# Kernel tuning notes

Hardware: AMD Instinct MI355X
Metric: run time of the kernel (lower is better)

The kernel has to match this reference:

```python
import jax, jax.numpy as jnp
import numpy as np

B, D, L = 32, 512, 4096   # batch, latent_dim (dim1), time length
N, D2 = 77, 768           # text tokens, text_latent_dim (dim2)
BC = 24                   # number of conditioned batch elements
H = 8                     # num_heads
EPS = 1e-5


def _layernorm(x, g, b):
    mu = jnp.mean(x, axis=-1, keepdims=True)
    var = jnp.mean(jnp.square(x - mu), axis=-1, keepdims=True)
    return (x - mu) * jax.lax.rsqrt(var + EPS) * g + b


def setup_inputs() -> dict:
    key = jax.random.key(0)
    ks = jax.random.split(key, 8)
    s = 0.02
    return {
        "input_tensor": jax.random.normal(ks[0], (B, D, L), jnp.float32),
        "condition_tensor": jax.random.normal(ks[1], (B, N, D2), jnp.float32),
        "cond_indices": jnp.arange(BC, dtype=jnp.int64 if jax.config.jax_enable_x64 else jnp.int32),
        "ln_g": jnp.ones((D,), jnp.float32),
        "ln_b": jnp.zeros((D,), jnp.float32),
        "tln_g": jnp.ones((D2,), jnp.float32),
        "tln_b": jnp.zeros((D2,), jnp.float32),
        "Wq": jax.random.normal(ks[2], (D, D), jnp.float32) * s,
        "bq": jnp.zeros((D,), jnp.float32),
        "Wk": jax.random.normal(ks[3], (D2, D), jnp.float32) * s,
        "bk": jnp.zeros((D,), jnp.float32),
        "Wv": jax.random.normal(ks[4], (D2, D), jnp.float32) * s,
        "bv": jnp.zeros((D,), jnp.float32),
    }


def reference(input_tensor, condition_tensor, cond_indices,
              ln_g, ln_b, tln_g, tln_b, Wq, bq, Wk, bk, Wv, bv):
    dh = D // H
    # gather conditioned rows; [Bc, D, L] -> [Bc, T=L, D]
    x_cond = jnp.transpose(input_tensor[cond_indices], (0, 2, 1))
    cond = condition_tensor[cond_indices]  # [Bc, N, D2]

    q = _layernorm(x_cond, ln_g, ln_b) @ Wq + bq           # [Bc, T, D]
    cn = _layernorm(cond, tln_g, tln_b)                     # [Bc, N, D2]
    k = (cn @ Wk + bk).reshape(BC, N, H, dh)
    v = (cn @ Wv + bv).reshape(BC, N, H, dh)

    q = jax.nn.softmax(q.reshape(BC, L, H, dh), axis=-1)   # feature-map softmax
    k = jax.nn.softmax(k, axis=1)                           # softmax over tokens N

    context = jnp.einsum('bnhk,bnhv->bhkv', k, v)           # [Bc, H, dh, dh]
    y = jnp.einsum('bthk,bhkv->bthv', q, context).reshape(BC, L, D)

    # scatter residual back: indices are unique, so .add == torch index assignment
    return input_tensor.at[cond_indices].add(jnp.transpose(y, (0, 2, 1)))
```

## Files before the change

kernel.cpp:

```cpp
#include <hip/hip_runtime.h>

#define LN_EPS 1e-5f

typedef __attribute__((ext_vector_type(8))) short bf16x8;
typedef __attribute__((ext_vector_type(4))) float f32x4;

__device__ __forceinline__ unsigned short f2bf(float f){
  unsigned u = __builtin_bit_cast(unsigned, f);
  u = (u + 0x7fffu + ((u >> 16) & 1u)) >> 16;
  return (unsigned short)u;
}
__device__ __forceinline__ float bf2f(unsigned short h){
  unsigned u = ((unsigned)h) << 16;
  return __builtin_bit_cast(float, u);
}

__global__ void k_prep(const float* __restrict__ Wq, const float* __restrict__ ln_g,
                       const float* __restrict__ ln_b, const float* __restrict__ bq,
                       unsigned short* __restrict__ gWqT, float2* __restrict__ c12)
{
  __shared__ float r1[64][4], r2[64][4];
  const int tid = threadIdx.x;
  const int n0 = blockIdx.x * 64;
  const int c = tid & 63, q = tid >> 6;
  const int n = n0 + c;
  float c1p = 0.f, c2p = 0.f;
  for(int i=0;i<128;i+=4){
    ushort4 pk;
    unsigned short* pp = (unsigned short*)&pk;
    #pragma unroll
    for(int j=0;j<4;j++){
      const int d = q*128 + i + j;
      const float wv = Wq[(size_t)d*512 + n];
      const unsigned short hb = f2bf(ln_g[d] * wv);
      pp[j] = hb;
      c2p += bf2f(hb);
      c1p += ln_b[d] * wv;
    }
    *(ushort4*)(gWqT + (size_t)n*512 + q*128 + i) = pk;
  }
  r1[c][q] = c1p; r2[c][q] = c2p;
  __syncthreads();
  if(q == 0){
    float a = 0.f, b2 = 0.f;
    #pragma unroll
    for(int j=0;j<4;j++){ a += r1[c][j]; b2 += r2[c][j]; }
    c12[n] = make_float2(a + bq[n], b2);
  }
}

__global__ void k_condkv(const float* __restrict__ cond, const int* __restrict__ idx,
                         const float* __restrict__ tg, const float* __restrict__ tb,
                         const float* __restrict__ Wk, const float* __restrict__ bk,
                         const float* __restrict__ Wv, const float* __restrict__ bv,
                         float* __restrict__ kbuf, float* __restrict__ vbuf)
{
  __shared__ float cn[16][768];
  const int bc = blockIdx.z, nc = blockIdx.y, dc = blockIdx.x;
  const int b = idx[bc];
  const int n0 = nc * 16;
  int nrows = 77 - n0; if(nrows > 16) nrows = 16;
  const int w = threadIdx.x >> 6, lane = threadIdx.x & 63;

  for(int r = w; r < nrows; r += 4){
    const float* src = cond + ((size_t)b * 77 + n0 + r) * 768;
    float vals[12]; float s1 = 0.f, s2 = 0.f;
    #pragma unroll
    for(int i=0;i<12;i++){ float x = src[lane + i*64]; vals[i]=x; s1+=x; s2+=x*x; }
    #pragma unroll
    for(int off=1; off<64; off<<=1){ s1 += __shfl_xor(s1, off); s2 += __shfl_xor(s2, off); }
    const float mu  = s1 * (1.f/768.f);
    const float var = s2 * (1.f/768.f) - mu*mu;
    const float rs  = rsqrtf(var + LN_EPS);
    #pragma unroll
    for(int i=0;i<12;i++){ const int c2 = lane + i*64; cn[r][c2] = (vals[i]-mu)*rs*tg[c2] + tb[c2]; }
  }
  __syncthreads();

  const int dq = threadIdx.x & 63;
  const int part = threadIdx.x >> 6;
  const float* W    = (dc < 2) ? Wk : Wv;
  const float* bias = (dc < 2) ? bk : bv;
  float* obuf       = (dc < 2) ? kbuf : vbuf;
  const int d0 = (dc & 1) * 256 + dq * 4;

  float acc[4][4] = {};
  for(int i=0;i<768;i++){
    const float4 wv = *(const float4*)(W + (size_t)i * 512 + d0);
    #pragma unroll
    for(int j=0;j<4;j++){
      const float c = cn[part*4 + j][i];
      acc[j][0] += c * wv.x; acc[j][1] += c * wv.y;
      acc[j][2] += c * wv.z; acc[j][3] += c * wv.w;
    }
  }
  #pragma unroll
  for(int j=0;j<4;j++){
    const int r = part*4 + j, n = n0 + r;
    if(r < nrows){
      float4 o;
      o.x = acc[j][0] + bias[d0+0];
      o.y = acc[j][1] + bias[d0+1];
      o.z = acc[j][2] + bias[d0+2];
      o.w = acc[j][3] + bias[d0+3];
      *(float4*)(obuf + ((size_t)bc * 77 + n) * 512 + d0) = o;
    }
  }
}

__global__ void k_ctx(const float* __restrict__ kbuf, const float* __restrict__ vbuf,
                      unsigned short* __restrict__ ctxP)
{
  __shared__ float kk[77][64];
  __shared__ float vv[77][64];
  __shared__ float inv_s[64];
  const int h = blockIdx.x, bc = blockIdx.y;
  const int tid = threadIdx.x;
  for(int e = tid; e < 77*64; e += 256){
    const int n = e >> 6, c = e & 63;
    kk[n][c] = kbuf[((size_t)bc * 77 + n) * 512 + h*64 + c];
    vv[n][c] = vbuf[((size_t)bc * 77 + n) * 512 + h*64 + c];
  }
  __syncthreads();
  if(tid < 64){
    float m = -1e30f;
    for(int n=0;n<77;n++) m = fmaxf(m, kk[n][tid]);
    float s = 0.f;
    for(int n=0;n<77;n++){ const float e = __expf(kk[n][tid] - m); kk[n][tid] = e; s += e; }
    inv_s[tid] = 1.f / s;
  }
  __syncthreads();
  #pragma unroll
  for(int j=0;j<16;j++){
    const int o = tid + 256*j;
    const int v = o >> 6, k2 = o & 63;
    float a = 0.f;
    for(int n=0;n<77;n++) a += kk[n][k2] * vv[n][v];
    const int pos = ((((k2>>5)*4 + (v>>4))*4 + ((k2>>3)&3))*16 + (v&15))*8 + (k2&7);
    ctxP[((size_t)(bc*8 + h)) * 4096 + pos] = f2bf(a * inv_s[k2]);
  }
}

__global__ __launch_bounds__(256, 3)
void k_fused(const float* __restrict__ input, const int* __restrict__ idx,
             const unsigned short* __restrict__ gWqT, const float2* __restrict__ c12,
             const unsigned short* __restrict__ ctxP, float* __restrict__ out)
{
  const int nt  = blockIdx.x;
  const int by  = blockIdx.y;
  const int tid = threadIdx.x;

  if(by >= 1536){
    const int cid = (by - 1536)*2 + nt;
    const int nb = cid >> 6, chunk = cid & 63;
    int cnt = 0, bsel = 0;
    for(int b2 = 0; b2 < 32; ++b2){
      bool member = false;
      #pragma unroll
      for(int i2 = 0; i2 < 24; ++i2) member |= (idx[i2] == b2);
      if(!member){ if(cnt == nb) bsel = b2; ++cnt; }
    }
    const float4* s = (const float4*)(input + (size_t)bsel * 2097152) + chunk*8192;
    float4*       d = (float4*)      (out   + (size_t)bsel * 2097152) + chunk*8192;
    #pragma unroll
    for(int i = 0; i < 32; ++i) d[i*256 + tid] = s[i*256 + tid];
    return;
  }

  __shared__ __align__(16) char smem[40960];
  unsigned short* const P = (unsigned short*)smem;
  float* const mu_s = (float*)(smem + 37376);
  float* const rs_s = (float*)(smem + 37632);
  float* const red1 = (float*)(smem + 37888);
  float* const red2 = (float*)(smem + 38912);

  const int lane = tid & 63, w = tid >> 6;
  const int col = lane & 15, g = lane >> 4;
  const int bc = by >> 6, b = idx[bc];
  const int t0 = (by & 63) * 64;
  const int nbase = nt * 256;
  const float* xb = input + (size_t)b * 2097152;

  const int tq = tid & 15;
  const int kb = tid >> 4;
  const float* xsrc = xb + (size_t)(kb*2) * 4096 + t0 + tq*4;

  int wx[4];
  #pragma unroll
  for(int j=0;j<4;j++){
    const int t = tq*4 + j;
    wx[j] = t*64 + ((((kb>>2) ^ ((t>>1)&3)) & 3) << 4) + ((kb & 3) << 2);
  }
  int offA[4];
  #pragma unroll
  for(int mt=0; mt<4; ++mt){
    const int row = mt*16 + col;
    offA[mt] = row*64 + ((g ^ ((row>>1)&3)) << 4);
  }
  const char* wrow[4];
  #pragma unroll
  for(int ntl=0; ntl<4; ++ntl)
    wrow[ntl] = (const char*)gWqT + (size_t)(nbase + w*64 + ntl*16 + col)*1024 + g*16;

  #define PUTX(ya, yb2, Xd)                                           \
  { _Pragma("unroll")                                                 \
    for(int j=0;j<4;j++)                                              \
      *(ushort2*)((Xd) + wx[j]) = make_ushort2(f2bf((&(ya).x)[j]), f2bf((&(yb2).x)[j])); }
  #define STATS(ya, yb2)                                              \
  { _Pragma("unroll")                                                 \
    for(int j=0;j<4;j++){                                             \
      const float a_ = (&(ya).x)[j], b_ = (&(yb2).x)[j];              \
      s1[j] += a_ + b_; s2[j] += a_*a_ + b_*b_; } }

  float s1[4] = {0,0,0,0}, s2[4] = {0,0,0,0};
  f32x4 acc[4][4] = {};

  {
    float4 xa  = *(const float4*)(xsrc);
    float4 xb2 = *(const float4*)(xsrc + 4096);
    STATS(xa, xb2);
    PUTX(xa, xb2, smem);
  }
  __syncthreads();

  for(int ks = 0; ks < 16; ++ks){
    char* const Xc = smem + ((ks & 1) << 12);
    char* const Xn = smem + (((ks + 1) & 1) << 12);
    float4 xa, xb2;
    const bool pf = (ks < 15);
    if(pf){
      xa  = *(const float4*)(xsrc + (size_t)((ks+1)*32) * 4096);
      xb2 = *(const float4*)(xsrc + (size_t)((ks+1)*32 + 1) * 4096);
    }
    bf16x8 bfr[4], af[4];
    #pragma unroll
    for(int ntl=0; ntl<4; ++ntl) bfr[ntl] = *(const bf16x8*)(wrow[ntl] + ks*64);
    #pragma unroll
    for(int mt=0; mt<4; ++mt) af[mt] = *(const bf16x8*)(Xc + offA[mt]);
    #pragma unroll
    for(int mt=0; mt<4; ++mt)
      #pragma unroll
      for(int ntl=0; ntl<4; ++ntl)
        acc[mt][ntl] = __builtin_amdgcn_mfma_f32_16x16x32_bf16(af[mt], bfr[ntl], acc[mt][ntl], 0, 0, 0);
    if(pf){
      STATS(xa, xb2);
      PUTX(xa, xb2, Xn);
    }
    __syncthreads();
  }
  #undef PUTX
  #undef STATS

  #pragma unroll
  for(int j=0;j<4;j++){
    s1[j] += __shfl_xor(s1[j], 16); s2[j] += __shfl_xor(s2[j], 16);
    s1[j] += __shfl_xor(s1[j], 32); s2[j] += __shfl_xor(s2[j], 32);
  }
  if(lane < 16){
    #pragma unroll
    for(int j=0;j<4;j++){
      red1[(lane*4 + j)*4 + w] = s1[j];
      red2[(lane*4 + j)*4 + w] = s2[j];
    }
  }
  __syncthreads();
  if(tid < 64){
    float a = 0.f, c = 0.f;
    #pragma unroll
    for(int ww=0; ww<4; ++ww){ a += red1[tid*4 + ww]; c += red2[tid*4 + ww]; }
    const float mu  = a * (1.f/512.f);
    const float var = c * (1.f/512.f) - mu*mu;
    mu_s[tid] = mu;
    rs_s[tid] = rsqrtf(var + LN_EPS);
  }
  __syncthreads();

  const int head = nt*4 + w;
  float c1b[4], c2v[4];
  #pragma unroll
  for(int ntl=0; ntl<4; ++ntl){
    const float2 cc = c12[nbase + w*64 + ntl*16 + col];
    c1b[ntl] = cc.x;
    c2v[ntl] = cc.y;
  }
  #pragma unroll
  for(int mt=0; mt<4; ++mt){
    #pragma unroll
    for(int r=0; r<4; ++r){
      const int tl = mt*16 + g*4 + r;
      const float rsr = rs_s[tl];
      const float mrc = rsr * mu_s[tl];
      float v[4];
      #pragma unroll
      for(int ntl=0; ntl<4; ++ntl)
        v[ntl] = rsr*acc[mt][ntl][r] - mrc*c2v[ntl] + c1b[ntl];
      float m = fmaxf(fmaxf(v[0],v[1]), fmaxf(v[2],v[3]));
      m = fmaxf(m, __shfl_xor(m, 1));
      m = fmaxf(m, __shfl_xor(m, 2));
      m = fmaxf(m, __shfl_xor(m, 4));
      m = fmaxf(m, __shfl_xor(m, 8));
      float s = 0.f;
      #pragma unroll
      for(int ntl=0; ntl<4; ++ntl){ v[ntl] = __expf(v[ntl] - m); s += v[ntl]; }
      s += __shfl_xor(s, 1);
      s += __shfl_xor(s, 2);
      s += __shfl_xor(s, 4);
      s += __shfl_xor(s, 8);
      const float inv = 1.f / s;
      #pragma unroll
      for(int ntl=0; ntl<4; ++ntl) acc[mt][ntl][r] = v[ntl] * inv;
    }
  }

  unsigned short* const Pw = P + w * (64*72);
  #pragma unroll
  for(int mt=0; mt<4; ++mt)
    #pragma unroll
    for(int ntl=0; ntl<4; ++ntl)
      #pragma unroll
      for(int r=0; r<4; ++r)
        Pw[(mt*16 + g*4 + r)*72 + ntl*16 + col] = f2bf(acc[mt][ntl][r]);

  const unsigned short* cp = ctxP + (size_t)(bc*8 + head) * 4096;
  f32x4 y[4][4] = {};
  #pragma unroll
  for(int ks2=0; ks2<2; ++ks2){
    bf16x8 pa[4];
    #pragma unroll
    for(int mt=0; mt<4; ++mt)
      pa[mt] = *(const bf16x8*)(Pw + (mt*16 + col)*72 + ks2*32 + g*8);
    bf16x8 cv[4];
    #pragma unroll
    for(int vt=0; vt<4; ++vt)
      cv[vt] = *(const bf16x8*)(cp + (size_t)(((ks2*4 + vt)*4 + g)*16 + col) * 8);
    #pragma unroll
    for(int mt=0; mt<4; ++mt)
      #pragma unroll
      for(int vt=0; vt<4; ++vt)
        y[mt][vt] = __builtin_amdgcn_mfma_f32_16x16x32_bf16(pa[mt], cv[vt], y[mt][vt], 0, 0, 0);
  }

  float* const ob = out + (size_t)b * 2097152;
  #pragma unroll
  for(int mt=0; mt<4; ++mt)
    #pragma unroll
    for(int vt=0; vt<4; ++vt){
      const size_t a = (size_t)(head*64 + vt*16 + col)*4096
                     + (size_t)(t0 + mt*16 + g*4);
      const float4 xr4 = *(const float4*)(xb + a);
      float4 o4;
      o4.x = xr4.x + y[mt][vt][0];
      o4.y = xr4.y + y[mt][vt][1];
      o4.z = xr4.z + y[mt][vt][2];
      o4.w = xr4.w + y[mt][vt][3];
      *(float4*)(ob + a) = o4;
    }
}

extern "C" void kernel_launch(void* const* d_in, const int* in_sizes, int n_in,
                              void* d_out, int out_size, void* d_ws, size_t ws_size,
                              hipStream_t stream)
{
  const float* input = (const float*)d_in[0];
  const float* cond  = (const float*)d_in[1];
  const int*   idx   = (const int*)d_in[2];
  const float* ln_g  = (const float*)d_in[3];
  const float* ln_b  = (const float*)d_in[4];
  const float* tln_g = (const float*)d_in[5];
  const float* tln_b = (const float*)d_in[6];
  const float* Wq    = (const float*)d_in[7];
  const float* bq    = (const float*)d_in[8];
  const float* Wk    = (const float*)d_in[9];
  const float* bk    = (const float*)d_in[10];
  const float* Wv    = (const float*)d_in[11];
  const float* bv    = (const float*)d_in[12];
  float* out = (float*)d_out;
  char*  ws  = (char*)d_ws;

  unsigned short* gWqT = (unsigned short*)(ws);
  float2*         c12  = (float2*)(ws + 524288);
  unsigned short* ctxP = (unsigned short*)(ws + 528384);
  float* kbuf = (float*)(ws + 2101248);
  float* vbuf = (float*)(ws + 2101248 + 3784704);

  k_prep  <<<dim3(8),       dim3(256), 0, stream>>>(Wq, ln_g, ln_b, bq, gWqT, c12);
  k_condkv<<<dim3(4,5,24),  dim3(256), 0, stream>>>(cond, idx, tln_g, tln_b, Wk, bk, Wv, bv, kbuf, vbuf);
  k_ctx   <<<dim3(8,24),    dim3(256), 0, stream>>>(kbuf, vbuf, ctxP);
  k_fused <<<dim3(2,1792),  dim3(256), 0, stream>>>(input, idx, gWqT, c12, ctxP, out);
}
```

Before: 416.6 us.

## Merge prep into cond-KV kernel and restructure fused GEMM X staging with K=64 steps

Folds the Wq preparation kernel into the cond K/V projection kernel as an extra z-slice, which removes one launch. Restructures the fused kernel's X tile loading: each thread now loads 16 scalar column elements per step, packs them into two 16-byte LDS writes with a new 8-way XOR swizzle, and processes K=64 per iteration (8 iterations instead of 16). This halves the number of barriers and lets each thread compute LN stats per row without shuffles. The trade-off is scalar strided global loads (coalesced across t) in place of float4 loads, plus a larger LDS footprint per buffer.

```diff
diff --git a/kernel.cpp b/kernel.cpp
--- a/kernel.cpp
+++ b/kernel.cpp
@@ -14,53 +14,61 @@
   unsigned u = ((unsigned)h) << 16;
   return __builtin_bit_cast(float, u);
 }
-
-__global__ void k_prep(const float* __restrict__ Wq, const float* __restrict__ ln_g,
-                       const float* __restrict__ ln_b, const float* __restrict__ bq,
-                       unsigned short* __restrict__ gWqT, float2* __restrict__ c12)
-{
-  __shared__ float r1[64][4], r2[64][4];
-  const int tid = threadIdx.x;
-  const int n0 = blockIdx.x * 64;
-  const int c = tid & 63, q = tid >> 6;
-  const int n = n0 + c;
-  float c1p = 0.f, c2p = 0.f;
-  for(int i=0;i<128;i+=4){
-    ushort4 pk;
-    unsigned short* pp = (unsigned short*)&pk;
-    #pragma unroll
-    for(int j=0;j<4;j++){
-      const int d = q*128 + i + j;
-      const float wv = Wq[(size_t)d*512 + n];
-      const unsigned short hb = f2bf(ln_g[d] * wv);
-      pp[j] = hb;
-      c2p += bf2f(hb);
-      c1p += ln_b[d] * wv;
-    }
-    *(ushort4*)(gWqT + (size_t)n*512 + q*128 + i) = pk;
-  }
-  r1[c][q] = c1p; r2[c][q] = c2p;
-  __syncthreads();
-  if(q == 0){
-    float a = 0.f, b2 = 0.f;
-    #pragma unroll
-    for(int j=0;j<4;j++){ a += r1[c][j]; b2 += r2[c][j]; }
-    c12[n] = make_float2(a + bq[n], b2);
-  }
-}
-
-__global__ void k_condkv(const float* __restrict__ cond, const int* __restrict__ idx,
-                         const float* __restrict__ tg, const float* __restrict__ tb,
-                         const float* __restrict__ Wk, const float* __restrict__ bk,
-                         const float* __restrict__ Wv, const float* __restrict__ bv,
-                         float* __restrict__ kbuf, float* __restrict__ vbuf)
+__device__ __forceinline__ unsigned pk2(float lo, float hi){
+  return (unsigned)f2bf(lo) | ((unsigned)f2bf(hi) << 16);
+}
+
+__global__ void k_aux(const float* __restrict__ Wq, const float* __restrict__ ln_g,
+                      const float* __restrict__ ln_b, const float* __restrict__ bq,
+                      unsigned short* __restrict__ gWqT, float2* __restrict__ c12,
+                      const float* __restrict__ cond, const int* __restrict__ idx,
+                      const float* __restrict__ tg, const float* __restrict__ tb,
+                      const float* __restrict__ Wk, const float* __restrict__ bk,
+                      const float* __restrict__ Wv, const float* __restrict__ bv,
+                      float* __restrict__ kbuf, float* __restrict__ vbuf)
 {
   __shared__ float cn[16][768];
+  const int tid = threadIdx.x;
+
+  if(blockIdx.z == 24){
+    const int pb = blockIdx.x + 4*blockIdx.y;
+    if(pb >= 8) return;
+    float* const r1 = &cn[0][0];
+    float* const r2 = &cn[0][0] + 256;
+    const int n0 = pb * 64;
+    const int c = tid & 63, q = tid >> 6;
+    const int n = n0 + c;
+    float c1p = 0.f, c2p = 0.f;
+    for(int i=0;i<128;i+=4){
+      ushort4 pkv;
+      unsigned short* pp = (unsigned short*)&pkv;
+      #pragma unroll
+      for(int j=0;j<4;j++){
+        const int d = q*128 + i + j;
+        const float wv = Wq[(size_t)d*512 + n];
+        const unsigned short hb = f2bf(ln_g[d] * wv);
+        pp[j] = hb;
+        c2p += bf2f(hb);
+        c1p += ln_b[d] * wv;
+      }
+      *(ushort4*)(gWqT + (size_t)n*512 + q*128 + i) = pkv;
+    }
+    r1[c*4 + q] = c1p; r2[c*4 + q] = c2p;
+    __syncthreads();
+    if(q == 0){
+      float a = 0.f, b2 = 0.f;
+      #pragma unroll
+      for(int j=0;j<4;j++){ a += r1[c*4+j]; b2 += r2[c*4+j]; }
+      c12[n] = make_float2(a + bq[n], b2);
+    }
+    return;
+  }
+
   const int bc = blockIdx.z, nc = blockIdx.y, dc = blockIdx.x;
   const int b = idx[bc];
   const int n0 = nc * 16;
   int nrows = 77 - n0; if(nrows > 16) nrows = 16;
-  const int w = threadIdx.x >> 6, lane = threadIdx.x & 63;
+  const int w = tid >> 6, lane = tid & 63;
 
   for(int r = w; r < nrows; r += 4){
     const float* src = cond + ((size_t)b * 77 + n0 + r) * 768;
@@ -77,8 +85,8 @@
   }
   __syncthreads();
 
-  const int dq = threadIdx.x & 63;
-  const int part = threadIdx.x >> 6;
+  const int dq = tid & 63;
+  const int part = tid >> 6;
   const float* W    = (dc < 2) ? Wk : Wv;
   const float* bias = (dc < 2) ? bk : bv;
   float* obuf       = (dc < 2) ? kbuf : vbuf;
@@ -169,10 +177,10 @@
 
   __shared__ __align__(16) char smem[40960];
   unsigned short* const P = (unsigned short*)smem;
-  float* const mu_s = (float*)(smem + 37376);
-  float* const rs_s = (float*)(smem + 37632);
-  float* const red1 = (float*)(smem + 37888);
-  float* const red2 = (float*)(smem + 38912);
+  float* const mu_s = (float*)(smem + 36864);
+  float* const rs_s = (float*)(smem + 37120);
+  float* const red1 = (float*)(smem + 37376);
+  float* const red2 = (float*)(smem + 38400);
 
   const int lane = tid & 63, w = tid >> 6;
   const int col = lane & 15, g = lane >> 4;
@@ -181,95 +189,100 @@
   const int nbase = nt * 256;
   const float* xb = input + (size_t)b * 2097152;
 
-  const int tq = tid & 15;
-  const int kb = tid >> 4;
-  const float* xsrc = xb + (size_t)(kb*2) * 4096 + t0 + tq*4;
-
-  int wx[4];
-  #pragma unroll
-  for(int j=0;j<4;j++){
-    const int t = tq*4 + j;
-    wx[j] = t*64 + ((((kb>>2) ^ ((t>>1)&3)) & 3) << 4) + ((kb & 3) << 2);
-  }
-  int offA[4];
-  #pragma unroll
-  for(int mt=0; mt<4; ++mt){
-    const int row = mt*16 + col;
-    offA[mt] = row*64 + ((g ^ ((row>>1)&3)) << 4);
-  }
+  const int t = tid & 63;
+  const int q = tid >> 6;
+  const float* xcol = xb + t0 + t;
+
+  const int wxA = t*128 + ((((q<<1)    ) ^ ((t>>1)&7)) << 4);
+  const int wxB = t*128 + ((((q<<1) | 1) ^ ((t>>1)&7)) << 4);
+
+  int offA[2][4];
+  #pragma unroll
+  for(int kk=0; kk<2; ++kk)
+    #pragma unroll
+    for(int mt=0; mt<4; ++mt){
+      const int row = mt*16 + col;
+      offA[kk][mt] = row*128 + (((kk*4 + g) ^ ((row>>1)&7)) << 4);
+    }
+
   const char* wrow[4];
   #pragma unroll
   for(int ntl=0; ntl<4; ++ntl)
     wrow[ntl] = (const char*)gWqT + (size_t)(nbase + w*64 + ntl*16 + col)*1024 + g*16;
 
-  #define PUTX(ya, yb2, Xd)                                           \
-  { _Pragma("unroll")                                                 \
-    for(int j=0;j<4;j++)                                              \
-      *(ushort2*)((Xd) + wx[j]) = make_ushort2(f2bf((&(ya).x)[j]), f2bf((&(yb2).x)[j])); }
-  #define STATS(ya, yb2)                                              \
-  { _Pragma("unroll")                                                 \
-    for(int j=0;j<4;j++){                                             \
-      const float a_ = (&(ya).x)[j], b_ = (&(yb2).x)[j];              \
-      s1[j] += a_ + b_; s2[j] += a_*a_ + b_*b_; } }
-
-  float s1[4] = {0,0,0,0}, s2[4] = {0,0,0,0};
+  float s1 = 0.f, s2 = 0.f;
   f32x4 acc[4][4] = {};
 
+  #define XLOAD(xv, ks)                                                       \
+  { _Pragma("unroll")                                                         \
+    for(int j=0;j<16;j++) xv[j] = xcol[(size_t)((ks)*64 + q*16 + j) * 4096]; }
+  #define XSTAT(xv)                                                           \
+  { _Pragma("unroll")                                                         \
+    for(int j=0;j<16;j++){ s1 += xv[j]; s2 += xv[j]*xv[j]; } }
+  #define XPUT(xv, Xd)                                                        \
+  { uint4 ua, ub;                                                             \
+    ua.x = pk2(xv[0],xv[1]);  ua.y = pk2(xv[2],xv[3]);                        \
+    ua.z = pk2(xv[4],xv[5]);  ua.w = pk2(xv[6],xv[7]);                        \
+    ub.x = pk2(xv[8],xv[9]);  ub.y = pk2(xv[10],xv[11]);                      \
+    ub.z = pk2(xv[12],xv[13]);ub.w = pk2(xv[14],xv[15]);                      \
+    *(uint4*)((Xd) + wxA) = ua;                                               \
+    *(uint4*)((Xd) + wxB) = ub; }
+
   {
-    float4 xa  = *(const float4*)(xsrc);
-    float4 xb2 = *(const float4*)(xsrc + 4096);
-    STATS(xa, xb2);
-    PUTX(xa, xb2, smem);
-  }
-  __syncthreads();
-
-  for(int ks = 0; ks < 16; ++ks){
-    char* const Xc = smem + ((ks & 1) << 12);
-    char* const Xn = smem + (((ks + 1) & 1) << 12);
-    float4 xa, xb2;
-    const bool pf = (ks < 15);
-    if(pf){
-      xa  = *(const float4*)(xsrc + (size_t)((ks+1)*32) * 4096);
-      xb2 = *(const float4*)(xsrc + (size_t)((ks+1)*32 + 1) * 4096);
-    }
-    bf16x8 bfr[4], af[4];
-    #pragma unroll
-    for(int ntl=0; ntl<4; ++ntl) bfr[ntl] = *(const bf16x8*)(wrow[ntl] + ks*64);
-    #pragma unroll
-    for(int mt=0; mt<4; ++mt) af[mt] = *(const bf16x8*)(Xc + offA[mt]);
-    #pragma unroll
-    for(int mt=0; mt<4; ++mt)
+    float xv[16];
+    XLOAD(xv, 0);
+    XSTAT(xv);
+    XPUT(xv, smem);
+  }
+  asm volatile("s_waitcnt lgkmcnt(0)" ::: "memory");
+  __builtin_amdgcn_s_barrier();
+
+  for(int ks = 0; ks < 8; ++ks){
+    char* const Xc = smem + ((ks & 1) << 13);
+    char* const Xn = smem + (((ks + 1) & 1) << 13);
+
+    float xn[16];
+    if(ks < 7){ XLOAD(xn, ks+1); }
+    bf16x8 wf[2][4];
+    #pragma unroll
+    for(int kk=0; kk<2; ++kk)
       #pragma unroll
       for(int ntl=0; ntl<4; ++ntl)
-        acc[mt][ntl] = __builtin_amdgcn_mfma_f32_16x16x32_bf16(af[mt], bfr[ntl], acc[mt][ntl], 0, 0, 0);
-    if(pf){
-      STATS(xa, xb2);
-      PUTX(xa, xb2, Xn);
-    }
-    __syncthreads();
-  }
-  #undef PUTX
-  #undef STATS
-
-  #pragma unroll
-  for(int j=0;j<4;j++){
-    s1[j] += __shfl_xor(s1[j], 16); s2[j] += __shfl_xor(s2[j], 16);
-    s1[j] += __shfl_xor(s1[j], 32); s2[j] += __shfl_xor(s2[j], 32);
-  }
-  if(lane < 16){
-    #pragma unroll
-    for(int j=0;j<4;j++){
-      red1[(lane*4 + j)*4 + w] = s1[j];
-      red2[(lane*4 + j)*4 + w] = s2[j];
-    }
-  }
+        wf[kk][ntl] = *(const bf16x8*)(wrow[ntl] + ks*128 + kk*64);
+
+    #pragma unroll
+    for(int kk=0; kk<2; ++kk){
+      bf16x8 af[4];
+      #pragma unroll
+      for(int mt=0; mt<4; ++mt) af[mt] = *(const bf16x8*)(Xc + offA[kk][mt]);
+      #pragma unroll
+      for(int ntl=0; ntl<4; ++ntl)
+        #pragma unroll
+        for(int mt=0; mt<4; ++mt)
+          acc[mt][ntl] = __builtin_amdgcn_mfma_f32_16x16x32_bf16(af[mt], wf[kk][ntl], acc[mt][ntl], 0, 0, 0);
+    }
+
+    __builtin_amdgcn_s_barrier();
+
+    if(ks < 7){
+      XSTAT(xn);
+      XPUT(xn, Xn);
+      asm volatile("s_waitcnt lgkmcnt(0)" ::: "memory");
+      __builtin_amdgcn_s_barrier();
+    }
+  }
+  #undef XLOAD
+  #undef XSTAT
+  #undef XPUT
+
+  red1[t*4 + q] = s1;
+  red2[t*4 + q] = s2;
   __syncthreads();
   if(tid < 64){
-    float a = 0.f, c = 0.f;
-    #pragma unroll
-    for(int ww=0; ww<4; ++ww){ a += red1[tid*4 + ww]; c += red2[tid*4 + ww]; }
+    const float a  = red1[tid*4] + red1[tid*4+1] + red1[tid*4+2] + red1[tid*4+3];
+    const float c2 = red2[tid*4] + red2[tid*4+1] + red2[tid*4+2] + red2[tid*4+3];
     const float mu  = a * (1.f/512.f);
-    const float var = c * (1.f/512.f) - mu*mu;
+    const float var = c2 * (1.f/512.f) - mu*mu;
     mu_s[tid] = mu;
     rs_s[tid] = rsqrtf(var + LN_EPS);
   }
@@ -383,8 +396,9 @@
   float* kbuf = (float*)(ws + 2101248);
   float* vbuf = (float*)(ws + 2101248 + 3784704);
 
-  k_prep  <<<dim3(8),       dim3(256), 0, stream>>>(Wq, ln_g, ln_b, bq, gWqT, c12);
-  k_condkv<<<dim3(4,5,24),  dim3(256), 0, stream>>>(cond, idx, tln_g, tln_b, Wk, bk, Wv, bv, kbuf, vbuf);
-  k_ctx   <<<dim3(8,24),    dim3(256), 0, stream>>>(kbuf, vbuf, ctxP);
-  k_fused <<<dim3(2,1792),  dim3(256), 0, stream>>>(input, idx, gWqT, c12, ctxP, out);
-}
+  k_aux  <<<dim3(4,5,25),  dim3(256), 0, stream>>>(Wq, ln_g, ln_b, bq, gWqT, c12,
+                                                   cond, idx, tln_g, tln_b,
+                                                   Wk, bk, Wv, bv, kbuf, vbuf);
+  k_ctx  <<<dim3(8,24),    dim3(256), 0, stream>>>(kbuf, vbuf, ctxP);
+  k_fused<<<dim3(2,1792),  dim3(256), 0, stream>>>(input, idx, gWqT, c12, ctxP, out);
+}
```

Measured after the change: 425.7 us. +2.2%, slower.
